# Kernel optimization log

Hardware: AMD Instinct MI355X
Metric: run time of the kernel (lower is better)

The kernel has to match this reference:

```python
import jax, jax.numpy as jnp
import numpy as np

Q_MAX = 6.0        # NVFP4 act mode
SCALE_MAX = 448.0  # scale clamp in manual_quant_act
BLOCK = 128        # forward passes self.block_size (128), not the fn default 16


def quant_act(x):
    # block-wise fake quant: reshape to (-1, BLOCK), per-block absmax scale,
    # round, clamp to [-Q_MAX, Q_MAX], rescale
    shp = x.shape
    xf = x.reshape(-1, BLOCK)
    raw_scale = jnp.clip(jnp.max(jnp.abs(xf), axis=-1, keepdims=True), 1e-12, None) / Q_MAX
    scale = jnp.minimum(raw_scale, SCALE_MAX)
    xq = jnp.clip(jnp.round(xf / scale), -Q_MAX, Q_MAX) * scale
    return xq.reshape(shp)


def setup_inputs() -> dict:
    key = jax.random.key(0)
    ks = jax.random.split(key, 6)
    B, S, D_IN, D_OUT, R = 4, 4096, 4096, 4096, 64
    x = jax.random.normal(ks[0], (B, S, D_IN), dtype=jnp.float32)
    w_ternary = jax.random.normal(ks[1], (D_OUT, D_IN), dtype=jnp.float32) * 0.02
    smooth_scale = jax.random.uniform(ks[2], (D_IN,), dtype=jnp.float32, minval=0.5, maxval=1.5)
    lora_a = jax.random.normal(ks[3], (R, D_IN), dtype=jnp.float32) * 0.02
    lora_b = jax.random.normal(ks[4], (D_OUT, R), dtype=jnp.float32) * 0.02
    bias = jax.random.normal(ks[5], (D_OUT,), dtype=jnp.float32) * 0.01
    return {"x": x, "w_ternary": w_ternary, "smooth_scale": smooth_scale,
            "lora_a": lora_a, "lora_b": lora_b, "bias": bias}


def reference(x, w_ternary, smooth_scale, lora_a, lora_b, bias):
    # smooth-scale activations, block fake-quant, base GEMM + low-rank SVD correction
    x_q = quant_act(x * smooth_scale)                      # [B,S,D_in]
    base_out = jnp.einsum('bsd,od->bso', x_q, w_ternary)   # [B,S,D_out]
    svd_out = jnp.einsum('bsr,or->bso',
                         jnp.einsum('bsd,rd->bsr', x_q, lora_a), lora_b)
    return base_out + svd_out + bias
```

## Files before the change

kernel.cpp:

```cpp
#include <hip/hip_runtime.h>
#include <hip/hip_bf16.h>

using short8 = __attribute__((ext_vector_type(8))) short;
using f32x4  = __attribute__((ext_vector_type(4))) float;

#define GLL16(g, l)                                                          \
  __builtin_amdgcn_global_load_lds(                                          \
      (const __attribute__((address_space(1))) void*)(g),                    \
      (__attribute__((address_space(3))) void*)(l), 16, 0, 0)

__global__ __launch_bounds__(256) void quant_kernel(
    const float* __restrict__ x, const float* __restrict__ smooth,
    __hip_bfloat16* __restrict__ xq, int D) {
  int tid = threadIdx.x;
  size_t qb = (size_t)blockIdx.x * 8 + (tid >> 5);
  int l = tid & 31;
  size_t base = qb * 128 + (size_t)l * 4;
  const float4 v = *(const float4*)(x + base);
  int d = (int)(base & (size_t)(D - 1));
  const float4 s = *(const float4*)(smooth + d);
  float y0 = v.x * s.x, y1 = v.y * s.y, y2 = v.z * s.z, y3 = v.w * s.w;
  float am = fmaxf(fmaxf(fabsf(y0), fabsf(y1)), fmaxf(fabsf(y2), fabsf(y3)));
#pragma unroll
  for (int off = 1; off < 32; off <<= 1)
    am = fmaxf(am, __shfl_xor(am, off, 64));
  float scale = fminf(fmaxf(am, 1e-12f) / 6.0f, 448.0f);
  float q0 = fminf(fmaxf(rintf(y0 / scale), -6.0f), 6.0f) * scale;
  float q1 = fminf(fmaxf(rintf(y1 / scale), -6.0f), 6.0f) * scale;
  float q2 = fminf(fmaxf(rintf(y2 / scale), -6.0f), 6.0f) * scale;
  float q3 = fminf(fmaxf(rintf(y3 / scale), -6.0f), 6.0f) * scale;
  union {
    __hip_bfloat16 h[4];
    uint2 u;
  } pk;
  pk.h[0] = __float2bfloat16(q0);
  pk.h[1] = __float2bfloat16(q1);
  pk.h[2] = __float2bfloat16(q2);
  pk.h[3] = __float2bfloat16(q3);
  *(uint2*)(xq + base) = pk.u;
}

__global__ __launch_bounds__(256) void wprep_kernel(
    const float* __restrict__ w, const float* __restrict__ la,
    const float* __restrict__ lb, __hip_bfloat16* __restrict__ weff, int Dk,
    int R) {
  __shared__ float lbs[16 * 64];
  int tid = threadIdx.x;
  int o0 = (blockIdx.x >> 4) * 16;
  int d = ((blockIdx.x & 15) << 8) + tid;
#pragma unroll
  for (int i = 0; i < 4; ++i) {
    int idx = tid + i * 256;
    lbs[idx] = lb[(size_t)(o0 + (idx >> 6)) * R + (idx & 63)];
  }
  __syncthreads();
  float acc[16];
#pragma unroll
  for (int oo = 0; oo < 16; ++oo) acc[oo] = 0.f;
  for (int r = 0; r < 64; ++r) {
    float av = la[(size_t)r * Dk + d];
#pragma unroll
    for (int oo = 0; oo < 16; ++oo) acc[oo] += lbs[oo * 64 + r] * av;
  }
#pragma unroll
  for (int oo = 0; oo < 16; ++oo) {
    size_t idx = (size_t)(o0 + oo) * Dk + d;
    weff[idx] = __float2bfloat16(w[idx] + acc[oo]);
  }
}

#define BM 256
#define BN 256
#define BKT 64

__global__ __launch_bounds__(512, 2) void gemm_kernel(
    const __hip_bfloat16* __restrict__ A, const __hip_bfloat16* __restrict__ B,
    const float* __restrict__ bias, float* __restrict__ C, int M, int N,
    int K) {
  __shared__ __attribute__((aligned(16))) char lds[131072];

  const int tid = threadIdx.x;
  const int wave = tid >> 6, lane = tid & 63;
  const int wr = wave >> 2, wc = wave & 3;
  const int lr = lane & 15;
  const int hi16 = (lane >> 4) * 16;
  const int swx = (lr & 7) << 4;

  const int nwg = gridDim.x;
  const int cpx = nwg >> 3;
  const int swzb = (blockIdx.x & 7) * cpx + (blockIdx.x >> 3);
  const int ntn = N / BN;
  const int tm = swzb / ntn, tn = swzb % ntn;
  const size_t m0 = (size_t)tm * BM, n0 = (size_t)tn * BN;

  const int trow = tid >> 3;
  const int csw = ((tid & 7) ^ (trow & 7)) * 8;
  const __hip_bfloat16* baseA = A + (m0 + trow) * (size_t)K + csw;
  const __hip_bfloat16* baseB = B + (n0 + trow) * (size_t)K + csw;
  char* sbase = lds + wave * 1024;

  const char* rdA = lds + (wr * 64 + lr) * 128;
  const char* rdB = lds + 32768 + (wc * 32 + lr) * 128;

#define STAGE(d, ab, h, kt)                                                   \
  do {                                                                        \
    const __hip_bfloat16* _g = ((ab) ? baseB : baseA) +                       \
                               (size_t)((h) * 128) * K + (size_t)(kt) * BKT;  \
    char* _l = sbase + (d) * 65536 + (ab) * 32768 + (h) * 16384;              \
    GLL16(_g, _l);                                                            \
    GLL16(_g + 64 * (size_t)K, _l + 8192);                                    \
  } while (0)

#define READ_A(DST, d, h)                                                     \
  _Pragma("unroll") for (int m = 0; m < 4; ++m)                               \
      _Pragma("unroll") for (int kk = 0; kk < 2; ++kk)                        \
          DST[m][kk] = *(const short8*)(rdA + (d) * 65536 + (h) * 16384 +     \
                                        m * 2048 + ((kk * 64 + hi16) ^ swx));

#define READ_B(DST, d, g)                                                     \
  _Pragma("unroll") for (int n = 0; n < 2; ++n)                               \
      _Pragma("unroll") for (int kk = 0; kk < 2; ++kk)                        \
          DST[n][kk] = *(const short8*)(rdB + (d) * 65536 + (g) * 16384 +     \
                                        n * 2048 + ((kk * 64 + hi16) ^ swx));

#define MFMA16(h, g, AF, BF)                                                  \
  _Pragma("unroll") for (int kk = 0; kk < 2; ++kk)                            \
      _Pragma("unroll") for (int m = 0; m < 4; ++m)                           \
          _Pragma("unroll") for (int n = 0; n < 2; ++n)                       \
              acc[h][m][g][n] = __builtin_amdgcn_mfma_f32_16x16x32_bf16(      \
                  AF[m][kk], BF[n][kk], acc[h][m][g][n], 0, 0, 0);

#define BARRIER __builtin_amdgcn_s_barrier()
#define SBAR0 __builtin_amdgcn_sched_barrier(0)
#define GATE                                                                  \
  asm volatile("s_waitcnt lgkmcnt(0)" ::: "memory");                          \
  __builtin_amdgcn_sched_barrier(0)
#define VMW6()                                                                \
  asm volatile("s_waitcnt vmcnt(6)" ::: "memory");                            \
  __builtin_amdgcn_sched_barrier(0)

  short8 aF0[4][2], aF1[4][2], bF0[2][2], bF1[2][2];
  f32x4 acc[2][4][2][2];
#pragma unroll
  for (int h = 0; h < 2; ++h)
#pragma unroll
    for (int m = 0; m < 4; ++m)
#pragma unroll
      for (int g = 0; g < 2; ++g)
#pragma unroll
        for (int n = 0; n < 2; ++n) acc[h][m][g][n] = (f32x4){0.f, 0.f, 0.f, 0.f};

  const int NK = K / BKT;

  STAGE(0, 0, 0, 0);
  STAGE(0, 1, 1, 0);
  STAGE(0, 0, 1, 0);
  STAGE(0, 1, 0, 0);
  STAGE(1, 0, 0, 1);
  STAGE(1, 1, 1, 1);
  STAGE(1, 0, 1, 1);
  VMW6();
  BARRIER;

  const int niter = NK / 2;
  for (int i = 0; i < niter; ++i) {
    const int k2 = (2 * i + 2 < NK) ? 2 * i + 2 : NK - 1;
    const int k3 = (2 * i + 3 < NK) ? 2 * i + 3 : NK - 1;
    READ_A(aF0, 0, 0);
    READ_B(bF0, 0, 0);
    STAGE(1, 1, 0, 2 * i + 1);
    BARRIER;
    GATE;
    __builtin_amdgcn_s_setprio(1);
    MFMA16(0, 0, aF0, bF0);
    __builtin_amdgcn_s_setprio(0);
    READ_B(bF1, 0, 1);
    SBAR0;
    BARRIER;
    STAGE(0, 0, 0, k2);
    BARRIER;
    GATE;
    __builtin_amdgcn_s_setprio(1);
    MFMA16(0, 1, aF0, bF1);
    __builtin_amdgcn_s_setprio(0);
    READ_A(aF1, 0, 1);
    SBAR0;
    BARRIER;
    STAGE(0, 1, 1, k2);
    BARRIER;
    GATE;
    __builtin_amdgcn_s_setprio(1);
    MFMA16(1, 1, aF1, bF1);
    __builtin_amdgcn_s_setprio(0);
    SBAR0;
    BARRIER;
    STAGE(0, 0, 1, k2);
    BARRIER;
    GATE;
    __builtin_amdgcn_s_setprio(1);
    MFMA16(1, 0, aF1, bF0);
    __builtin_amdgcn_s_setprio(0);
    VMW6();
    SBAR0;
    BARRIER;
    READ_A(aF0, 1, 0);
    READ_B(bF0, 1, 0);
    STAGE(0, 1, 0, k2);
    BARRIER;
    GATE;
    __builtin_amdgcn_s_setprio(1);
    MFMA16(0, 0, aF0, bF0);
    __builtin_amdgcn_s_setprio(0);
    READ_B(bF1, 1, 1);
    SBAR0;
    BARRIER;
    STAGE(1, 0, 0, k3);
    BARRIER;
    GATE;
    __builtin_amdgcn_s_setprio(1);
    MFMA16(0, 1, aF0, bF1);
    __builtin_amdgcn_s_setprio(0);
    READ_A(aF1, 1, 1);
    SBAR0;
    BARRIER;
    STAGE(1, 1, 1, k3);
    BARRIER;
    GATE;
    __builtin_amdgcn_s_setprio(1);
    MFMA16(1, 1, aF1, bF1);
    __builtin_amdgcn_s_setprio(0);
    SBAR0;
    BARRIER;
    STAGE(1, 0, 1, k3);
    BARRIER;
    GATE;
    __builtin_amdgcn_s_setprio(1);
    MFMA16(1, 0, aF1, bF0);
    __builtin_amdgcn_s_setprio(0);
    VMW6();
    SBAR0;
    BARRIER;
  }

#pragma unroll
  for (int h = 0; h < 2; ++h)
#pragma unroll
    for (int g = 0; g < 2; ++g)
#pragma unroll
      for (int n = 0; n < 2; ++n) {
        const int col = (int)n0 + g * 128 + wc * 32 + n * 16 + lr;
        const float bv = bias[col];
#pragma unroll
        for (int m = 0; m < 4; ++m) {
          const int row = (int)m0 + h * 128 + wr * 64 + m * 16 + (lane >> 4) * 4;
#pragma unroll
          for (int r = 0; r < 4; ++r)
            C[(size_t)(row + r) * N + col] = acc[h][m][g][n][r] + bv;
        }
      }
}

extern "C" void kernel_launch(void* const* d_in, const int* in_sizes, int n_in,
                              void* d_out, int out_size, void* d_ws,
                              size_t ws_size, hipStream_t stream) {
  const float* x = (const float*)d_in[0];
  const float* w = (const float*)d_in[1];
  const float* smooth = (const float*)d_in[2];
  const float* la = (const float*)d_in[3];
  const float* lb = (const float*)d_in[4];
  const float* bias = (const float*)d_in[5];
  float* out = (float*)d_out;

  const int K = in_sizes[2];
  const int N = in_sizes[5];
  const int M = in_sizes[0] / K;
  const int R = in_sizes[3] / K;

  __hip_bfloat16* xq = (__hip_bfloat16*)d_ws;
  __hip_bfloat16* weff = xq + (size_t)M * K;

  {
    size_t qblocks = ((size_t)M * K) / 128;
    int blocks = (int)(qblocks / 8);
    quant_kernel<<<blocks, 256, 0, stream>>>(x, smooth, xq, K);
  }
  {
    int blocks = (N / 16) * (K / 256);
    wprep_kernel<<<blocks, 256, 0, stream>>>(w, la, lb, weff, K, R);
  }
  {
    int blocks = (M / BM) * (N / BN);
    gemm_kernel<<<blocks, 512, 0, stream>>>(xq, weff, bias, out, M, N, K);
  }
}
```

Measured before the change: 629.7 us.

## Switch GEMM to 32x32x16 MFMA with k-major LDS layout

Replaces the 16x16x32 bf16 MFMA tiling with 32x32x16 MFMA instructions. The LDS staging layout changes from row-major swizzled to a k-chunk-major layout, so each lane reads contiguous 16-byte chunks without XOR swizzle. The aim is fewer MFMA issues and fewer LDS reads per tile. Global loads now fetch 16-byte column chunks per row, which makes global access less coalesced, and the new LDS layout may introduce bank conflicts.

```diff
diff --git a/kernel.cpp b/kernel.cpp
--- a/kernel.cpp
+++ b/kernel.cpp
@@ -3,6 +3,7 @@
 
 using short8 = __attribute__((ext_vector_type(8))) short;
 using f32x4  = __attribute__((ext_vector_type(4))) float;
+using f32x16 = __attribute__((ext_vector_type(16))) float;
 
 #define GLL16(g, l)                                                          \
   __builtin_amdgcn_global_load_lds(                                          \
@@ -82,9 +83,8 @@
   const int tid = threadIdx.x;
   const int wave = tid >> 6, lane = tid & 63;
   const int wr = wave >> 2, wc = wave & 3;
-  const int lr = lane & 15;
-  const int hi16 = (lane >> 4) * 16;
-  const int swx = (lr & 7) << 4;
+  const int l31 = lane & 31;
+  const int ksel = lane >> 5;
 
   const int nwg = gridDim.x;
   const int cpx = nwg >> 3;
@@ -93,14 +93,14 @@
   const int tm = swzb / ntn, tn = swzb % ntn;
   const size_t m0 = (size_t)tm * BM, n0 = (size_t)tn * BN;
 
-  const int trow = tid >> 3;
-  const int csw = ((tid & 7) ^ (trow & 7)) * 8;
-  const __hip_bfloat16* baseA = A + (m0 + trow) * (size_t)K + csw;
-  const __hip_bfloat16* baseB = B + (n0 + trow) * (size_t)K + csw;
+  const int stg_row = (wave & 1) * 64 + lane;
+  const int stg_c0 = (wave >> 1) * 8;
+  const __hip_bfloat16* baseA = A + (m0 + stg_row) * (size_t)K + stg_c0;
+  const __hip_bfloat16* baseB = B + (n0 + stg_row) * (size_t)K + stg_c0;
   char* sbase = lds + wave * 1024;
 
-  const char* rdA = lds + (wr * 64 + lr) * 128;
-  const char* rdB = lds + 32768 + (wc * 32 + lr) * 128;
+  const char* rdA = lds + ksel * 2048 + (wr * 64 + l31) * 16;
+  const char* rdB = lds + 32768 + ksel * 2048 + (wc * 32 + l31) * 16;
 
 #define STAGE(d, ab, h, kt)                                                   \
   do {                                                                        \
@@ -108,27 +108,24 @@
                                (size_t)((h) * 128) * K + (size_t)(kt) * BKT;  \
     char* _l = sbase + (d) * 65536 + (ab) * 32768 + (h) * 16384;              \
     GLL16(_g, _l);                                                            \
-    GLL16(_g + 64 * (size_t)K, _l + 8192);                                    \
+    GLL16(_g + 32, _l + 8192);                                                \
   } while (0)
 
-#define READ_A(DST, d, h)                                                     \
-  _Pragma("unroll") for (int m = 0; m < 4; ++m)                               \
-      _Pragma("unroll") for (int kk = 0; kk < 2; ++kk)                        \
-          DST[m][kk] = *(const short8*)(rdA + (d) * 65536 + (h) * 16384 +     \
-                                        m * 2048 + ((kk * 64 + hi16) ^ swx));
-
-#define READ_B(DST, d, g)                                                     \
-  _Pragma("unroll") for (int n = 0; n < 2; ++n)                               \
-      _Pragma("unroll") for (int kk = 0; kk < 2; ++kk)                        \
-          DST[n][kk] = *(const short8*)(rdB + (d) * 65536 + (g) * 16384 +     \
-                                        n * 2048 + ((kk * 64 + hi16) ^ swx));
-
-#define MFMA16(h, g, AF, BF)                                                  \
-  _Pragma("unroll") for (int kk = 0; kk < 2; ++kk)                            \
-      _Pragma("unroll") for (int m = 0; m < 4; ++m)                           \
-          _Pragma("unroll") for (int n = 0; n < 2; ++n)                       \
-              acc[h][m][g][n] = __builtin_amdgcn_mfma_f32_16x16x32_bf16(      \
-                  AF[m][kk], BF[n][kk], acc[h][m][g][n], 0, 0, 0);
+#define READ_A32(DST, d, h)                                                   \
+  _Pragma("unroll") for (int t2 = 0; t2 < 2; ++t2)                            \
+      _Pragma("unroll") for (int kk = 0; kk < 4; ++kk)                        \
+          DST[t2][kk] = *(const short8*)(rdA + (d) * 65536 + (h) * 16384 +    \
+                                         kk * 4096 + t2 * 512);
+
+#define READ_B32(DST, d, g)                                                   \
+  _Pragma("unroll") for (int kk = 0; kk < 4; ++kk)                            \
+      DST[kk] = *(const short8*)(rdB + (d) * 65536 + (g) * 16384 + kk * 4096);
+
+#define MFMA8(h, g, AF, BF)                                                   \
+  _Pragma("unroll") for (int kk = 0; kk < 4; ++kk)                            \
+      _Pragma("unroll") for (int t2 = 0; t2 < 2; ++t2)                        \
+          acc[h][t2][g] = __builtin_amdgcn_mfma_f32_32x32x16_bf16(            \
+              AF[t2][kk], BF[kk], acc[h][t2][g], 0, 0, 0);
 
 #define BARRIER __builtin_amdgcn_s_barrier()
 #define SBAR0 __builtin_amdgcn_sched_barrier(0)
@@ -139,16 +136,16 @@
   asm volatile("s_waitcnt vmcnt(6)" ::: "memory");                            \
   __builtin_amdgcn_sched_barrier(0)
 
-  short8 aF0[4][2], aF1[4][2], bF0[2][2], bF1[2][2];
-  f32x4 acc[2][4][2][2];
+  short8 aF0[2][4], aF1[2][4], bF0[4], bF1[4];
+  f32x16 acc[2][2][2];
 #pragma unroll
   for (int h = 0; h < 2; ++h)
 #pragma unroll
-    for (int m = 0; m < 4; ++m)
+    for (int t2 = 0; t2 < 2; ++t2)
 #pragma unroll
       for (int g = 0; g < 2; ++g)
 #pragma unroll
-        for (int n = 0; n < 2; ++n) acc[h][m][g][n] = (f32x4){0.f, 0.f, 0.f, 0.f};
+        for (int r = 0; r < 16; ++r) acc[h][t2][g][r] = 0.f;
 
   const int NK = K / BKT;
 
@@ -166,31 +163,31 @@
   for (int i = 0; i < niter; ++i) {
     const int k2 = (2 * i + 2 < NK) ? 2 * i + 2 : NK - 1;
     const int k3 = (2 * i + 3 < NK) ? 2 * i + 3 : NK - 1;
-    READ_A(aF0, 0, 0);
-    READ_B(bF0, 0, 0);
+    READ_A32(aF0, 0, 0);
+    READ_B32(bF0, 0, 0);
     STAGE(1, 1, 0, 2 * i + 1);
     BARRIER;
     GATE;
     __builtin_amdgcn_s_setprio(1);
-    MFMA16(0, 0, aF0, bF0);
-    __builtin_amdgcn_s_setprio(0);
-    READ_B(bF1, 0, 1);
+    MFMA8(0, 0, aF0, bF0);
+    __builtin_amdgcn_s_setprio(0);
+    READ_B32(bF1, 0, 1);
     SBAR0;
     BARRIER;
     STAGE(0, 0, 0, k2);
     BARRIER;
     GATE;
     __builtin_amdgcn_s_setprio(1);
-    MFMA16(0, 1, aF0, bF1);
-    __builtin_amdgcn_s_setprio(0);
-    READ_A(aF1, 0, 1);
+    MFMA8(0, 1, aF0, bF1);
+    __builtin_amdgcn_s_setprio(0);
+    READ_A32(aF1, 0, 1);
     SBAR0;
     BARRIER;
     STAGE(0, 1, 1, k2);
     BARRIER;
     GATE;
     __builtin_amdgcn_s_setprio(1);
-    MFMA16(1, 1, aF1, bF1);
+    MFMA8(1, 1, aF1, bF1);
     __builtin_amdgcn_s_setprio(0);
     SBAR0;
     BARRIER;
@@ -198,36 +195,36 @@
     BARRIER;
     GATE;
     __builtin_amdgcn_s_setprio(1);
-    MFMA16(1, 0, aF1, bF0);
+    MFMA8(1, 0, aF1, bF0);
     __builtin_amdgcn_s_setprio(0);
     VMW6();
     SBAR0;
     BARRIER;
-    READ_A(aF0, 1, 0);
-    READ_B(bF0, 1, 0);
+    READ_A32(aF0, 1, 0);
+    READ_B32(bF0, 1, 0);
     STAGE(0, 1, 0, k2);
     BARRIER;
     GATE;
     __builtin_amdgcn_s_setprio(1);
-    MFMA16(0, 0, aF0, bF0);
-    __builtin_amdgcn_s_setprio(0);
-    READ_B(bF1, 1, 1);
+    MFMA8(0, 0, aF0, bF0);
+    __builtin_amdgcn_s_setprio(0);
+    READ_B32(bF1, 1, 1);
     SBAR0;
     BARRIER;
     STAGE(1, 0, 0, k3);
     BARRIER;
     GATE;
     __builtin_amdgcn_s_setprio(1);
-    MFMA16(0, 1, aF0, bF1);
-    __builtin_amdgcn_s_setprio(0);
-    READ_A(aF1, 1, 1);
+    MFMA8(0, 1, aF0, bF1);
+    __builtin_amdgcn_s_setprio(0);
+    READ_A32(aF1, 1, 1);
     SBAR0;
     BARRIER;
     STAGE(1, 1, 1, k3);
     BARRIER;
     GATE;
     __builtin_amdgcn_s_setprio(1);
-    MFMA16(1, 1, aF1, bF1);
+    MFMA8(1, 1, aF1, bF1);
     __builtin_amdgcn_s_setprio(0);
     SBAR0;
     BARRIER;
@@ -235,7 +232,7 @@
     BARRIER;
     GATE;
     __builtin_amdgcn_s_setprio(1);
-    MFMA16(1, 0, aF1, bF0);
+    MFMA8(1, 0, aF1, bF0);
     __builtin_amdgcn_s_setprio(0);
     VMW6();
     SBAR0;
@@ -245,17 +242,16 @@
 #pragma unroll
   for (int h = 0; h < 2; ++h)
 #pragma unroll
-    for (int g = 0; g < 2; ++g)
-#pragma unroll
-      for (int n = 0; n < 2; ++n) {
-        const int col = (int)n0 + g * 128 + wc * 32 + n * 16 + lr;
+    for (int t2 = 0; t2 < 2; ++t2)
+#pragma unroll
+      for (int g = 0; g < 2; ++g) {
+        const int col = (int)n0 + g * 128 + wc * 32 + l31;
         const float bv = bias[col];
-#pragma unroll
-        for (int m = 0; m < 4; ++m) {
-          const int row = (int)m0 + h * 128 + wr * 64 + m * 16 + (lane >> 4) * 4;
-#pragma unroll
-          for (int r = 0; r < 4; ++r)
-            C[(size_t)(row + r) * N + col] = acc[h][m][g][n][r] + bv;
+        const int row0 = (int)m0 + h * 128 + wr * 64 + t2 * 32 + ksel * 4;
+#pragma unroll
+        for (int r = 0; r < 16; ++r) {
+          const int row = row0 + (r & 3) + 8 * (r >> 2);
+          C[(size_t)row * N + col] = acc[h][t2][g][r] + bv;
         }
       }
 }
```

New measurement: 790.1 us. 25.5% more time.
